# Kernel tuning notes

Hardware: AMD Instinct MI355X
Metric: run time of the kernel (lower is better)

Reference implementation:

```python
import jax, jax.numpy as jnp
import numpy as np

# Hierarchy: 3 levels with 50 / 500 / 5000 classes, branching factor 10.
PIQUETS = (0, 50, 550, 5550)  # cumulative offsets per level
NB_LEVELS = 3
BATCH = 4096


def _make_parent():
    """parent[j] = global index of the parent of global node j (0 for roots).
    Encodes the same structure as the dense H matrix (H[p, j] = 1 iff parent[j] == p)."""
    parent = np.zeros(PIQUETS[-1], dtype=np.int32)
    parent[PIQUETS[1]:PIQUETS[2]] = np.arange(500) // 10            # level-1 -> level-0
    parent[PIQUETS[2]:PIQUETS[3]] = PIQUETS[1] + np.arange(5000) // 10  # level-2 -> level-1
    return jnp.asarray(parent)


def setup_inputs() -> dict:
    key = jax.random.key(0)
    k1, k2 = jax.random.split(key)
    y_pred = jax.random.normal(k1, (BATCH, PIQUETS[-1]), dtype=jnp.float32)
    target = jax.random.randint(k2, (BATCH,), 0, 5000)  # local leaf-level indices
    return {"y_pred": y_pred, "target": target, "parent": _make_parent()}


def reference(y_pred, target, parent):
    # children_preds[b, p] = sum of child logits of node p
    # == (H[:piquets[-2], :] @ y_pred.T).T, exploiting H's one-parent sparsity.
    children = jax.ops.segment_sum(
        y_pred.T[PIQUETS[1]:], parent[PIQUETS[1]:], num_segments=PIQUETS[-2]
    ).T  # (B, piquets[-2])

    levels_pred = [y_pred[:, PIQUETS[k]:PIQUETS[k + 1]] for k in range(NB_LEVELS)]
    levels_children = [children[:, PIQUETS[k]:PIQUETS[k + 1]] for k in range(NB_LEVELS - 1)]
    log_p = [jax.nn.log_softmax(l, axis=1) for l in levels_pred]
    log_c = [jax.nn.log_softmax(l, axis=1) for l in levels_children]

    # Ancestor targets per level (vectorized replacement for get_grandparents loops)
    g = target.astype(jnp.int32) + PIQUETS[-2]  # global leaf index
    globs = [g]
    for _ in range(NB_LEVELS - 1):
        globs.append(parent[globs[-1]])
    globs = globs[::-1]  # level 0 .. level L-1, global indices
    loc = [globs[k] - PIQUETS[k] for k in range(NB_LEVELS)]  # local per-level targets

    def ce(logp, tgt):
        return -jnp.take_along_axis(logp, tgt[:, None], axis=1).mean()

    def kl_mean(logp, logq):
        # torch KLDivLoss(reduction='mean'): mean over ALL elements of q*(log q - log p)
        return jnp.mean(jnp.exp(logq) * (logq - logp))

    loss = jnp.float32(0.0)
    kl_penalty = jnp.float32(0.0)
    for k in range(NB_LEVELS - 1):
        kl_penalty += 0.5 * (kl_mean(log_p[k], log_c[k]) + kl_mean(log_c[k], log_p[k]))
        loss += 0.5 * ce(log_p[k], loc[k])
    loss += 0.5 * ce(log_p[-1], loc[-1])
    loss += 0.5 * kl_penalty
    return loss
```

## Files before the change

kernel.cpp:

```cpp
#include <hip/hip_runtime.h>

#define BATCH 4096
#define ROW   5550

__device__ __forceinline__ void lse_combine(float& m, float& s, float m2, float s2) {
    float mn = fmaxf(m, m2);
    s = s * __expf(m - mn) + s2 * __expf(m2 - mn);
    m = mn;
}

__device__ __forceinline__ void wave_lse(float& m, float& s) {
    #pragma unroll
    for (int off = 32; off; off >>= 1) {
        float m2 = __shfl_xor(m, off, 64);
        float s2 = __shfl_xor(s, off, 64);
        lse_combine(m, s, m2, s2);
    }
}

__device__ __forceinline__ float wave_sum(float v) {
    #pragma unroll
    for (int off = 32; off; off >>= 1) v += __shfl_xor(v, off, 64);
    return v;
}

__global__ __launch_bounds__(256)
void hjsd_kernel(const float* __restrict__ y, const int* __restrict__ tgt,
                 float* __restrict__ rowout) {
    __shared__ float s_row[ROW];
    __shared__ float s_c1[500];
    __shared__ float s_scr[48];

    const int b   = blockIdx.x;
    const int tid = threadIdx.x;

    const float2* prow  = reinterpret_cast<const float2*>(y + (size_t)b * ROW);
    float2*       srow2 = reinterpret_cast<float2*>(s_row);
    for (int i = tid; i < ROW / 2; i += 256) srow2[i] = prow[i];
    __syncthreads();

    float m2 = -1e30f, s2 = 0.0f;
    float mc1 = -1e30f, sc1 = 0.0f;
    if (tid < 250) {
        const float2* p = reinterpret_cast<const float2*>(s_row + 550 + 20 * tid);
        float v[20];
        #pragma unroll
        for (int j = 0; j < 10; ++j) { float2 t2 = p[j]; v[2*j] = t2.x; v[2*j+1] = t2.y; }
        float c0 = 0.f, c1 = 0.f, mx0 = -1e30f, mx1 = -1e30f;
        #pragma unroll
        for (int j = 0; j < 10; ++j) { c0 += v[j];      mx0 = fmaxf(mx0, v[j]); }
        #pragma unroll
        for (int j = 0; j < 10; ++j) { c1 += v[10 + j]; mx1 = fmaxf(mx1, v[10 + j]); }
        float se0 = 0.f, se1 = 0.f;
        #pragma unroll
        for (int j = 0; j < 10; ++j) se0 += __expf(v[j]      - mx0);
        #pragma unroll
        for (int j = 0; j < 10; ++j) se1 += __expf(v[10 + j] - mx1);
        lse_combine(m2, s2, mx0, se0);
        lse_combine(m2, s2, mx1, se1);
        s_c1[2 * tid]     = c0;
        s_c1[2 * tid + 1] = c1;
        mc1 = fmaxf(c0, c1);
        sc1 = __expf(c0 - mc1) + __expf(c1 - mc1);
    }

    float x1[10];
    float m1 = -1e30f, s1 = 0.0f, mc0 = -1e30f, sc0 = 0.0f;
    float c0v = 0.0f, x0 = 0.0f;
    if (tid < 50) {
        const float2* p = reinterpret_cast<const float2*>(s_row + 50 + 10 * tid);
        #pragma unroll
        for (int j = 0; j < 5; ++j) { float2 t2 = p[j]; x1[2*j] = t2.x; x1[2*j+1] = t2.y; }
        float sum = 0.f, mx = -1e30f;
        #pragma unroll
        for (int j = 0; j < 10; ++j) { sum += x1[j]; mx = fmaxf(mx, x1[j]); }
        float se = 0.f;
        #pragma unroll
        for (int j = 0; j < 10; ++j) se += __expf(x1[j] - mx);
        m1 = mx; s1 = se;
        c0v = sum;
        mc0 = sum; sc0 = 1.0f;
        x0 = s_row[tid];
    }
    float m0 = (tid < 50) ? x0 : -1e30f;
    float s0 = (tid < 50) ? 1.0f : 0.0f;

    wave_lse(m2, s2); wave_lse(mc1, sc1); wave_lse(m1, s1);
    wave_lse(mc0, sc0); wave_lse(m0, s0);
    const int wid = tid >> 6;
    if ((tid & 63) == 0) {
        float* w = s_scr + wid * 10;
        w[0] = m2;  w[1] = s2;
        w[2] = mc1; w[3] = sc1;
        w[4] = m1;  w[5] = s1;
        w[6] = mc0; w[7] = sc0;
        w[8] = m0;  w[9] = s0;
    }
    __syncthreads();
    float L[5];
    #pragma unroll
    for (int k = 0; k < 5; ++k) {
        float M = s_scr[2 * k], S = s_scr[2 * k + 1];
        lse_combine(M, S, s_scr[10 + 2 * k], s_scr[11 + 2 * k]);
        lse_combine(M, S, s_scr[20 + 2 * k], s_scr[21 + 2 * k]);
        lse_combine(M, S, s_scr[30 + 2 * k], s_scr[31 + 2 * k]);
        L[k] = M + __logf(S);
    }

    float part = 0.0f;
    if (tid < 50) {
        const float L2v = L[0], LC1 = L[1], L1v = L[2], LC0 = L[3], L0v = L[4];
        (void)L2v;
        float S11 = 0.f, S21 = 0.f;
        #pragma unroll
        for (int j = 0; j < 10; ++j) {
            float x = x1[j];
            float c = s_c1[10 * tid + j];
            S11 += __expf(c - LC1) * (c - x);
            S21 += __expf(x - L1v) * (x - c);
        }
        float S10 = __expf(c0v - LC0) * (c0v - x0);
        float S20 = __expf(x0  - L0v) * (x0 - c0v);
        part = (0.25f / 500.0f) * (S11 + S21) + (0.25f / 50.0f) * (S10 + S20);
    }
    __syncthreads();
    part = wave_sum(part);
    if ((tid & 63) == 0) s_scr[tid >> 6] = part;
    __syncthreads();

    if (tid == 0) {
        float Ssum = s_scr[0] + s_scr[1] + s_scr[2] + s_scr[3];
        int t = tgt[b];
        float ce0 = L[4] - s_row[t / 100];
        float ce1 = L[2] - s_row[50 + t / 10];
        float ce2 = L[0] - s_row[550 + t];
        rowout[b] = 0.5f * (ce0 + ce1 + ce2) + Ssum;
    }
}

__global__ __launch_bounds__(256)
void reduce_kernel(const float* __restrict__ rows, float* __restrict__ out) {
    __shared__ float scr[4];
    const int tid = threadIdx.x;
    const float4* p = reinterpret_cast<const float4*>(rows);
    float s = 0.0f;
    for (int i = tid; i < BATCH / 4; i += 256) {
        float4 v = p[i];
        s += v.x + v.y + v.z + v.w;
    }
    s = wave_sum(s);
    if ((tid & 63) == 0) scr[tid >> 6] = s;
    __syncthreads();
    if (tid == 0) out[0] = (scr[0] + scr[1] + scr[2] + scr[3]) * (1.0f / BATCH);
}

extern "C" void kernel_launch(void* const* d_in, const int* in_sizes, int n_in,
                              void* d_out, int out_size, void* d_ws, size_t ws_size,
                              hipStream_t stream) {
    const float* y   = (const float*)d_in[0];
    const int*   tgt = (const int*)d_in[1];
    float* out    = (float*)d_out;
    float* rowbuf = (float*)d_ws;

    hjsd_kernel<<<BATCH, 256, 0, stream>>>(y, tgt, rowbuf);
    reduce_kernel<<<1, 256, 0, stream>>>(rowbuf, out);
}
```

Baseline: 150.3 us.

## Use unshifted exp sums for single-pass LSE and KL, pad leaf smem layout

Replaces the max-tracking log-sum-exp reductions with plain sums of exp, and rewrites the KL terms as ratios of exp-weighted sums. Nine quantities are now reduced in one pass, which drops a barrier and the second KL loop. The row is scattered into three shared arrays per level, with the leaf array padded every 20 elements to cut bank conflicts on the float2 reads. Skipping the max subtraction trades numerical safety for speed: large logits, especially the 100-element child sums at level 0, could overflow exp.

```diff
diff --git a/kernel.cpp b/kernel.cpp
--- a/kernel.cpp
+++ b/kernel.cpp
@@ -2,21 +2,6 @@
 
 #define BATCH 4096
 #define ROW   5550
-
-__device__ __forceinline__ void lse_combine(float& m, float& s, float m2, float s2) {
-    float mn = fmaxf(m, m2);
-    s = s * __expf(m - mn) + s2 * __expf(m2 - mn);
-    m = mn;
-}
-
-__device__ __forceinline__ void wave_lse(float& m, float& s) {
-    #pragma unroll
-    for (int off = 32; off; off >>= 1) {
-        float m2 = __shfl_xor(m, off, 64);
-        float s2 = __shfl_xor(s, off, 64);
-        lse_combine(m, s, m2, s2);
-    }
-}
 
 __device__ __forceinline__ float wave_sum(float v) {
     #pragma unroll
@@ -27,114 +12,91 @@
 __global__ __launch_bounds__(256)
 void hjsd_kernel(const float* __restrict__ y, const int* __restrict__ tgt,
                  float* __restrict__ rowout) {
-    __shared__ float s_row[ROW];
-    __shared__ float s_c1[500];
-    __shared__ float s_scr[48];
+    __shared__ __align__(16) float s0[56];
+    __shared__ __align__(16) float s1[504];
+    __shared__ __align__(16) float s2[5504];
+    __shared__ float scr[36];
 
     const int b   = blockIdx.x;
     const int tid = threadIdx.x;
 
-    const float2* prow  = reinterpret_cast<const float2*>(y + (size_t)b * ROW);
-    float2*       srow2 = reinterpret_cast<float2*>(s_row);
-    for (int i = tid; i < ROW / 2; i += 256) srow2[i] = prow[i];
+    const float2* prow = reinterpret_cast<const float2*>(y + (size_t)b * ROW);
+    for (int i = tid; i < ROW / 2; i += 256) {
+        float2 v = prow[i];
+        int e = 2 * i;
+        if (e >= 550) {
+            int f   = e - 550;
+            int idx = f + 2 * (f / 20);
+            s2[idx] = v.x; s2[idx + 1] = v.y;
+        } else if (e >= 50) {
+            s1[e - 50] = v.x; s1[e - 49] = v.y;
+        } else {
+            s0[e] = v.x; s0[e + 1] = v.y;
+        }
+    }
     __syncthreads();
 
-    float m2 = -1e30f, s2 = 0.0f;
-    float mc1 = -1e30f, sc1 = 0.0f;
+    float E2 = 0.f, EC1 = 0.f, E1 = 0.f, EC0 = 0.f, E0 = 0.f;
+    float S11 = 0.f, S21 = 0.f, S10 = 0.f, S20 = 0.f;
+
     if (tid < 250) {
-        const float2* p = reinterpret_cast<const float2*>(s_row + 550 + 20 * tid);
+        const float2* p2 = reinterpret_cast<const float2*>(s2 + 22 * tid);
         float v[20];
         #pragma unroll
-        for (int j = 0; j < 10; ++j) { float2 t2 = p[j]; v[2*j] = t2.x; v[2*j+1] = t2.y; }
-        float c0 = 0.f, c1 = 0.f, mx0 = -1e30f, mx1 = -1e30f;
+        for (int j = 0; j < 10; ++j) { float2 t2 = p2[j]; v[2*j] = t2.x; v[2*j+1] = t2.y; }
+        float c0 = 0.f, c1 = 0.f;
         #pragma unroll
-        for (int j = 0; j < 10; ++j) { c0 += v[j];      mx0 = fmaxf(mx0, v[j]); }
+        for (int j = 0; j < 10; ++j) c0 += v[j];
         #pragma unroll
-        for (int j = 0; j < 10; ++j) { c1 += v[10 + j]; mx1 = fmaxf(mx1, v[10 + j]); }
-        float se0 = 0.f, se1 = 0.f;
+        for (int j = 0; j < 10; ++j) c1 += v[10 + j];
         #pragma unroll
-        for (int j = 0; j < 10; ++j) se0 += __expf(v[j]      - mx0);
-        #pragma unroll
-        for (int j = 0; j < 10; ++j) se1 += __expf(v[10 + j] - mx1);
-        lse_combine(m2, s2, mx0, se0);
-        lse_combine(m2, s2, mx1, se1);
-        s_c1[2 * tid]     = c0;
-        s_c1[2 * tid + 1] = c1;
-        mc1 = fmaxf(c0, c1);
-        sc1 = __expf(c0 - mc1) + __expf(c1 - mc1);
+        for (int j = 0; j < 20; ++j) E2 += __expf(v[j]);
+        float ec0 = __expf(c0), ec1 = __expf(c1);
+        EC1 = ec0 + ec1;
+        float xa = s1[2 * tid], xb = s1[2 * tid + 1];
+        float ea = __expf(xa), eb = __expf(xb);
+        E1  = ea + eb;
+        S11 = ec0 * (c0 - xa) + ec1 * (c1 - xb);
+        S21 = ea * (xa - c0) + eb * (xb - c1);
     }
 
-    float x1[10];
-    float m1 = -1e30f, s1 = 0.0f, mc0 = -1e30f, sc0 = 0.0f;
-    float c0v = 0.0f, x0 = 0.0f;
     if (tid < 50) {
-        const float2* p = reinterpret_cast<const float2*>(s_row + 50 + 10 * tid);
+        const float2* p1 = reinterpret_cast<const float2*>(s1 + 10 * tid);
+        float c = 0.f;
         #pragma unroll
-        for (int j = 0; j < 5; ++j) { float2 t2 = p[j]; x1[2*j] = t2.x; x1[2*j+1] = t2.y; }
-        float sum = 0.f, mx = -1e30f;
-        #pragma unroll
-        for (int j = 0; j < 10; ++j) { sum += x1[j]; mx = fmaxf(mx, x1[j]); }
-        float se = 0.f;
-        #pragma unroll
-        for (int j = 0; j < 10; ++j) se += __expf(x1[j] - mx);
-        m1 = mx; s1 = se;
-        c0v = sum;
-        mc0 = sum; sc0 = 1.0f;
-        x0 = s_row[tid];
+        for (int j = 0; j < 5; ++j) { float2 t2 = p1[j]; c += t2.x + t2.y; }
+        float ec = __expf(c);
+        float x0 = s0[tid];
+        float e0 = __expf(x0);
+        EC0 = ec; E0 = e0;
+        S10 = ec * (c - x0);
+        S20 = e0 * (x0 - c);
     }
-    float m0 = (tid < 50) ? x0 : -1e30f;
-    float s0 = (tid < 50) ? 1.0f : 0.0f;
 
-    wave_lse(m2, s2); wave_lse(mc1, sc1); wave_lse(m1, s1);
-    wave_lse(mc0, sc0); wave_lse(m0, s0);
+    float sums[9] = {E2, EC1, E1, EC0, E0, S11, S21, S10, S20};
+    #pragma unroll
+    for (int k = 0; k < 9; ++k) sums[k] = wave_sum(sums[k]);
     const int wid = tid >> 6;
     if ((tid & 63) == 0) {
-        float* w = s_scr + wid * 10;
-        w[0] = m2;  w[1] = s2;
-        w[2] = mc1; w[3] = sc1;
-        w[4] = m1;  w[5] = s1;
-        w[6] = mc0; w[7] = sc0;
-        w[8] = m0;  w[9] = s0;
+        #pragma unroll
+        for (int k = 0; k < 9; ++k) scr[wid * 9 + k] = sums[k];
     }
-    __syncthreads();
-    float L[5];
-    #pragma unroll
-    for (int k = 0; k < 5; ++k) {
-        float M = s_scr[2 * k], S = s_scr[2 * k + 1];
-        lse_combine(M, S, s_scr[10 + 2 * k], s_scr[11 + 2 * k]);
-        lse_combine(M, S, s_scr[20 + 2 * k], s_scr[21 + 2 * k]);
-        lse_combine(M, S, s_scr[30 + 2 * k], s_scr[31 + 2 * k]);
-        L[k] = M + __logf(S);
-    }
-
-    float part = 0.0f;
-    if (tid < 50) {
-        const float L2v = L[0], LC1 = L[1], L1v = L[2], LC0 = L[3], L0v = L[4];
-        (void)L2v;
-        float S11 = 0.f, S21 = 0.f;
-        #pragma unroll
-        for (int j = 0; j < 10; ++j) {
-            float x = x1[j];
-            float c = s_c1[10 * tid + j];
-            S11 += __expf(c - LC1) * (c - x);
-            S21 += __expf(x - L1v) * (x - c);
-        }
-        float S10 = __expf(c0v - LC0) * (c0v - x0);
-        float S20 = __expf(x0  - L0v) * (x0 - c0v);
-        part = (0.25f / 500.0f) * (S11 + S21) + (0.25f / 50.0f) * (S10 + S20);
-    }
-    __syncthreads();
-    part = wave_sum(part);
-    if ((tid & 63) == 0) s_scr[tid >> 6] = part;
     __syncthreads();
 
     if (tid == 0) {
-        float Ssum = s_scr[0] + s_scr[1] + s_scr[2] + s_scr[3];
+        float t9[9];
+        #pragma unroll
+        for (int k = 0; k < 9; ++k)
+            t9[k] = scr[k] + scr[9 + k] + scr[18 + k] + scr[27 + k];
+        float L2 = __logf(t9[0]), L1 = __logf(t9[2]), L0 = __logf(t9[4]);
         int t = tgt[b];
-        float ce0 = L[4] - s_row[t / 100];
-        float ce1 = L[2] - s_row[50 + t / 10];
-        float ce2 = L[0] - s_row[550 + t];
-        rowout[b] = 0.5f * (ce0 + ce1 + ce2) + Ssum;
+        float y2 = s2[t + 2 * (t / 20)];
+        float y1 = s1[t / 10];
+        float y0 = s0[t / 100];
+        float ce = (L2 - y2) + (L1 - y1) + (L0 - y0);
+        float kl = (0.25f / 500.0f) * (t9[5] / t9[1] + t9[6] / t9[2])
+                 + (0.25f / 50.0f)  * (t9[7] / t9[3] + t9[8] / t9[4]);
+        rowout[b] = 0.5f * ce + kl;
     }
 }
 
```

Result: faster. 146.9 us (-2.2%).
